# Kernel tuning notes

Measured on AMD Instinct MI355X. Metric: run time of the kernel, lower is better.

## Reference

```python
import jax, jax.numpy as jnp
import numpy as np


def setup_inputs() -> dict:
    key = jax.random.key(0)
    k1, k2 = jax.random.split(key)
    B, T, D = 32, 512, 384
    x = jax.random.normal(k1, (B, T, D), dtype=jnp.float32)
    duration = jax.random.randint(k2, (B, T), 0, 8, dtype=jnp.int64)
    max_len = 2048
    return {"x": x, "duration": duration, "max_len": max_len}


def reference(x, duration, max_len):
    # x: [B, T, D] phoneme-level features; duration: [B, T] int frame counts.
    # Frame j of utterance b copies phoneme i where cumsum(dur)[i-1] <= j < cumsum(dur)[i].
    B, T, D = x.shape
    cum = jnp.cumsum(duration, axis=1)                      # [B, T] exclusive upper bounds
    pos = jnp.arange(max_len)                               # [L]
    # searchsorted(side='right') maps frame index -> source phoneme index
    idx = jax.vmap(lambda c: jnp.searchsorted(c, pos, side="right"))(cum)  # [B, L]
    mel_len = cum[:, -1]                                    # [B] true expanded lengths
    valid = pos[None, :] < mel_len[:, None]                 # [B, L] pad mask
    idx_c = jnp.clip(idx, 0, T - 1)
    out = jnp.take_along_axis(x, idx_c[:, :, None], axis=1) # [B, L, D] gather
    out = jnp.where(valid[:, :, None], out, jnp.zeros((), dtype=x.dtype))
    return out, mel_len
```

## Files before the change

### kernel.cpp

```cpp
#include <hip/hip_runtime.h>


#define T_IN   512
#define D_DIM  384
#define D4     (D_DIM / 4)
#define MAXLEN 2048
#define B_SZ   32
#define ROWS_PER_BLOCK 16

__global__ __launch_bounds__(T_IN) void lr_scan_kernel(const int* __restrict__ dur,
                                                       int* __restrict__ cum_ws,
                                                       float* __restrict__ mel_out) {
    __shared__ int s[T_IN];
    const int b = blockIdx.x;
    const int t = threadIdx.x;
    s[t] = dur[b * T_IN + t];
    __syncthreads();
    #pragma unroll
    for (int off = 1; off < T_IN; off <<= 1) {
        int v = s[t];
        int add = (t >= off) ? s[t - off] : 0;
        __syncthreads();
        s[t] = v + add;
        __syncthreads();
    }
    cum_ws[b * T_IN + t] = s[t];
    if (t == T_IN - 1) mel_out[b] = (float)s[t];
}

__global__ __launch_bounds__(256) void lr_gather_kernel(const float* __restrict__ x,
                                                        const int* __restrict__ cum_ws,
                                                        float* __restrict__ out) {
    __shared__ int scum[T_IN];
    __shared__ int sidx[ROWS_PER_BLOCK];
    const int b = blockIdx.y;
    const int tid = threadIdx.x;

    const int* crow = cum_ws + b * T_IN;
    scum[tid] = crow[tid];
    scum[tid + 256] = crow[tid + 256];
    __syncthreads();

    if (tid < ROWS_PER_BLOCK) {
        const int p = blockIdx.x * ROWS_PER_BLOCK + tid;
        const int mel = scum[T_IN - 1];
        int lo = 0, hi = T_IN;
        while (lo < hi) {
            int mid = (lo + hi) >> 1;
            if (scum[mid] <= p) lo = mid + 1; else hi = mid;
        }
        if (lo > T_IN - 1) lo = T_IN - 1;
        sidx[tid] = (p < mel) ? lo : -1;
    }
    __syncthreads();

    const float4* __restrict__ x4 = (const float4*)x;
    float4* __restrict__ out4 =
        (float4*)out + ((size_t)b * MAXLEN + (size_t)blockIdx.x * ROWS_PER_BLOCK) * D4;
    #pragma unroll
    for (int i = 0; i < 6; ++i) {
        int flat = i * 256 + tid;
        int row = flat / D4;
        int chunk = flat - row * D4;
        int idx = sidx[row];
        float4 v = make_float4(0.f, 0.f, 0.f, 0.f);
        if (idx >= 0)
            v = x4[((size_t)b * T_IN + idx) * D4 + chunk];
        out4[flat] = v;
    }
}

extern "C" void kernel_launch(void* const* d_in, const int* in_sizes, int n_in,
                              void* d_out, int out_size, void* d_ws, size_t ws_size,
                              hipStream_t stream) {
    const float* x = (const float*)d_in[0];
    const int* dur = (const int*)d_in[1];

    float* out = (float*)d_out;
    float* mel_out = out + (size_t)B_SZ * MAXLEN * D_DIM;
    int* cum_ws = (int*)d_ws;

    lr_scan_kernel<<<B_SZ, T_IN, 0, stream>>>(dur, cum_ws, mel_out);

    dim3 grid(MAXLEN / ROWS_PER_BLOCK, B_SZ);
    lr_gather_kernel<<<grid, 256, 0, stream>>>(x, cum_ws, out);
}
```

Before: 29.81 us.

## Fuse duration scan into gather kernel and use nontemporal output stores

Removes the separate scan kernel launch and its workspace round-trip. Each gather block now recomputes the prefix sum of its utterance's durations in shared memory, using a 256-thread scan over paired elements. Output writes switch to nontemporal stores so the large streaming output does not pollute cache. The cost is redundant scan work in every block: 128 blocks per batch each repeat the same 8-step scan with barriers.

```diff
diff --git a/kernel.cpp b/kernel.cpp
--- a/kernel.cpp
+++ b/kernel.cpp
@@ -8,42 +8,40 @@
 #define B_SZ   32
 #define ROWS_PER_BLOCK 16
 
-__global__ __launch_bounds__(T_IN) void lr_scan_kernel(const int* __restrict__ dur,
-                                                       int* __restrict__ cum_ws,
+typedef float f32x4 __attribute__((ext_vector_type(4)));
+
+__global__ __launch_bounds__(256) void lr_fused_kernel(const float* __restrict__ x,
+                                                       const int* __restrict__ dur,
+                                                       float* __restrict__ out,
                                                        float* __restrict__ mel_out) {
-    __shared__ int s[T_IN];
-    const int b = blockIdx.x;
-    const int t = threadIdx.x;
-    s[t] = dur[b * T_IN + t];
-    __syncthreads();
-    #pragma unroll
-    for (int off = 1; off < T_IN; off <<= 1) {
-        int v = s[t];
-        int add = (t >= off) ? s[t - off] : 0;
-        __syncthreads();
-        s[t] = v + add;
-        __syncthreads();
-    }
-    cum_ws[b * T_IN + t] = s[t];
-    if (t == T_IN - 1) mel_out[b] = (float)s[t];
-}
-
-__global__ __launch_bounds__(256) void lr_gather_kernel(const float* __restrict__ x,
-                                                        const int* __restrict__ cum_ws,
-                                                        float* __restrict__ out) {
     __shared__ int scum[T_IN];
+    __shared__ int sp[256];
     __shared__ int sidx[ROWS_PER_BLOCK];
     const int b = blockIdx.y;
     const int tid = threadIdx.x;
 
-    const int* crow = cum_ws + b * T_IN;
-    scum[tid] = crow[tid];
-    scum[tid + 256] = crow[tid + 256];
+    int2 d2 = ((const int2*)(dur + b * T_IN))[tid];
+    const int pair = d2.x + d2.y;
+    sp[tid] = pair;
     __syncthreads();
+    #pragma unroll
+    for (int off = 1; off < 256; off <<= 1) {
+        int v = sp[tid];
+        int add = (tid >= off) ? sp[tid - off] : 0;
+        __syncthreads();
+        sp[tid] = v + add;
+        __syncthreads();
+    }
+    const int excl = sp[tid] - pair;
+    scum[2 * tid]     = excl + d2.x;
+    scum[2 * tid + 1] = excl + d2.x + d2.y;
+    __syncthreads();
+
+    const int mel = scum[T_IN - 1];
+    if (blockIdx.x == 0 && tid == 0) mel_out[b] = (float)mel;
 
     if (tid < ROWS_PER_BLOCK) {
         const int p = blockIdx.x * ROWS_PER_BLOCK + tid;
-        const int mel = scum[T_IN - 1];
         int lo = 0, hi = T_IN;
         while (lo < hi) {
             int mid = (lo + hi) >> 1;
@@ -54,19 +52,19 @@
     }
     __syncthreads();
 
-    const float4* __restrict__ x4 = (const float4*)x;
-    float4* __restrict__ out4 =
-        (float4*)out + ((size_t)b * MAXLEN + (size_t)blockIdx.x * ROWS_PER_BLOCK) * D4;
+    const f32x4* __restrict__ x4 = (const f32x4*)x;
+    f32x4* __restrict__ out4 =
+        (f32x4*)out + ((size_t)b * MAXLEN + (size_t)blockIdx.x * ROWS_PER_BLOCK) * D4;
     #pragma unroll
     for (int i = 0; i < 6; ++i) {
         int flat = i * 256 + tid;
         int row = flat / D4;
         int chunk = flat - row * D4;
         int idx = sidx[row];
-        float4 v = make_float4(0.f, 0.f, 0.f, 0.f);
+        f32x4 v = (f32x4)(0.f);
         if (idx >= 0)
             v = x4[((size_t)b * T_IN + idx) * D4 + chunk];
-        out4[flat] = v;
+        __builtin_nontemporal_store(v, &out4[flat]);
     }
 }
 
@@ -78,10 +76,7 @@
 
     float* out = (float*)d_out;
     float* mel_out = out + (size_t)B_SZ * MAXLEN * D_DIM;
-    int* cum_ws = (int*)d_ws;
-
-    lr_scan_kernel<<<B_SZ, T_IN, 0, stream>>>(dur, cum_ws, mel_out);
 
     dim3 grid(MAXLEN / ROWS_PER_BLOCK, B_SZ);
-    lr_gather_kernel<<<grid, 256, 0, stream>>>(x, cum_ws, out);
+    lr_fused_kernel<<<grid, 256, 0, stream>>>(x, dur, out, mel_out);
 }
```

Result: faster. 24.65 us (-17.3%).
